# Kernel tuning notes

Hardware: AMD Instinct MI355X
Metric: run time of the kernel (lower is better)

Reference implementation:

```python
import jax, jax.numpy as jnp
import numpy as np

N_NODES = 50000
N_EDGES = 800000
F_IN = 128
HID = 256


def setup_inputs() -> dict:
    key = jax.random.key(0)
    ks = jax.random.split(key, 10)
    x = jax.random.normal(ks[0], (N_NODES, F_IN), jnp.float32)
    edge_index = jax.random.randint(ks[1], (2, N_EDGES), 0, N_NODES, jnp.int32)
    # Glorot-ish scaled weights (PyG Linear default init style)
    def w(k, o, i):
        return jax.random.normal(k, (o, i), jnp.float32) * (1.0 / np.sqrt(i))
    return {
        "x": x,
        "edge_index": edge_index,
        "W1l": w(ks[2], HID, F_IN), "b1l": jnp.zeros((HID,), jnp.float32),
        "W1r": w(ks[3], HID, F_IN),
        "W2l": w(ks[4], HID, HID), "b2l": jnp.zeros((HID,), jnp.float32),
        "W2r": w(ks[5], HID, HID),
        "Wh1": w(ks[6], 4, HID), "bh1": jnp.zeros((4,), jnp.float32),
        "Wh2": w(ks[7], 3, HID), "bh2": jnp.zeros((3,), jnp.float32),
    }


def sage_conv(x, edge_index, Wl, bl, Wr):
    # PyG SAGEConv (aggr='mean'): out_i = Wl @ mean_{j in N(i)} x_j + bl + Wr @ x_i
    src, dst = edge_index[0], edge_index[1]
    n = x.shape[0]
    summed = jax.ops.segment_sum(x[src], dst, num_segments=n)        # [N, F]
    cnt = jax.ops.segment_sum(jnp.ones((src.shape[0],), x.dtype), dst, num_segments=n)
    agg = summed / jnp.maximum(cnt, 1.0)[:, None]                    # isolated nodes -> 0
    return agg @ Wl.T + bl + x @ Wr.T


def reference(x, edge_index, W1l, b1l, W1r, W2l, b2l, W2r, Wh1, bh1, Wh2, bh2):
    h = jax.nn.relu(sage_conv(x, edge_index, W1l, b1l, W1r))
    # dropout(p=0.5) is identity in eval mode
    h = sage_conv(h, edge_index, W2l, b2l, W2r)
    out1 = h @ Wh1.T + bh1   # l2_classifier=False branch
    out2 = h @ Wh2.T + bh2
    return (out1, out2, h)
```

## Files before the change

### kernel.cpp

```cpp
#include <hip/hip_runtime.h>
#include <hip/hip_bf16.h>

typedef short bf16x8 __attribute__((ext_vector_type(8)));
typedef float f32x4 __attribute__((ext_vector_type(4)));

__device__ __forceinline__ float bf2f(__hip_bfloat16 v) { return __bfloat162float(v); }
__device__ __forceinline__ float sh2f(short s) {
    union { float f; unsigned u; } c; c.u = ((unsigned)(unsigned short)s) << 16; return c.f;
}
__device__ __forceinline__ short f2sh(float f) {
    __hip_bfloat16 b = __float2bfloat16(f); return *(short*)&b;
}

__device__ __forceinline__ float loadAny(const void* p, size_t i, int isf32) {
    return isf32 ? ((const float*)p)[i] : bf2f(((const __hip_bfloat16*)p)[i]);
}

__global__ void pre_kernel(const void* __restrict__ x,
                           const void* W1l, const void* W1r, const void* W2l, const void* W2r,
                           const void* b1l, const void* b2l, const void* Wh1, const void* Wh2,
                           const void* bh1, const void* bh2,
                           const int* __restrict__ ei, int E,
                           __hip_bfloat16* __restrict__ xn,
                           __hip_bfloat16* __restrict__ W1c, __hip_bfloat16* __restrict__ W2c,
                           __hip_bfloat16* __restrict__ sb,
                           int* __restrict__ deg, int* __restrict__ rank,
                           int* __restrict__ flag, int N) {
    __shared__ int sflag;
    int tid = threadIdx.x;
    if (tid < 64) {
        const unsigned short* xu = (const unsigned short*)x;
        unsigned short u = xu[tid * 2];
        unsigned e = (u >> 7) & 0xFF;
        bool good = (u == 0) || (e >= 110 && e <= 137);
        unsigned long long m = __ballot(good);
        if (tid == 0) sflag = (__popcll(m) < 32) ? 1 : 0;
    }
    __syncthreads();
    int isf32 = sflag;
    int gid = blockIdx.x * 256 + tid;
    if (gid == 0) *flag = isf32;

    if (gid < E) {
        rank[gid] = atomicAdd(&deg[ei[E + gid]], 1);
    }

    int n4 = N * 32;
    if (gid < n4) {
        short4 o;
        if (isf32) {
            float4 v = ((const float4*)x)[gid];
            o.x = f2sh(v.x); o.y = f2sh(v.y); o.z = f2sh(v.z); o.w = f2sh(v.w);
        } else {
            o = ((const short4*)x)[gid];
        }
        ((short4*)xn)[gid] = o;
    }

    if (gid < 65536) {
        int n = gid >> 8, k = gid & 255;
        float v = (k < 128) ? loadAny(W1l, n * 128 + k, isf32)
                            : loadAny(W1r, n * 128 + (k - 128), isf32);
        W1c[gid] = __float2bfloat16(v);
        return;
    }
    int u = gid - 65536;
    if (u < 131072) {
        int n = u >> 9, k = u & 511;
        float v = (k < 256) ? loadAny(W2l, n * 256 + k, isf32)
                            : loadAny(W2r, n * 256 + (k - 256), isf32);
        W2c[u] = __float2bfloat16(v);
        return;
    }
    int s = u - 131072;
    float v;
    if      (s < 256)  v = loadAny(b1l, s, isf32);
    else if (s < 512)  v = loadAny(b2l, s - 256, isf32);
    else if (s < 1536) v = loadAny(Wh1, s - 512, isf32);
    else if (s < 2304) v = loadAny(Wh2, s - 1536, isf32);
    else if (s < 2308) v = loadAny(bh1, s - 2304, isf32);
    else if (s < 2311) v = loadAny(bh2, s - 2308, isf32);
    else return;
    sb[s] = __float2bfloat16(v);
}

__global__ __launch_bounds__(256) void scanA_kernel(const int* __restrict__ deg,
                                                    int* __restrict__ off,
                                                    int* __restrict__ bsum, int N) {
    __shared__ int ts[256];
    int t = threadIdx.x;
    int base = blockIdx.x * 1024 + t * 4;
    int v0 = (base + 0 < N) ? deg[base + 0] : 0;
    int v1 = (base + 1 < N) ? deg[base + 1] : 0;
    int v2 = (base + 2 < N) ? deg[base + 2] : 0;
    int v3 = (base + 3 < N) ? deg[base + 3] : 0;
    int i0 = v0, i1 = i0 + v1, i2 = i1 + v2, i3 = i2 + v3;
    ts[t] = i3;
    __syncthreads();
    for (int d = 1; d < 256; d <<= 1) {
        int x = (t >= d) ? ts[t - d] : 0;
        __syncthreads();
        ts[t] += x;
        __syncthreads();
    }
    int excl = (t > 0) ? ts[t - 1] : 0;
    if (base + 0 < N) off[base + 1] = excl + i0;
    if (base + 1 < N) off[base + 2] = excl + i1;
    if (base + 2 < N) off[base + 3] = excl + i2;
    if (base + 3 < N) off[base + 4] = excl + i3;
    if (t == 255) bsum[blockIdx.x] = ts[255];
}

__global__ void addC_kernel(int* __restrict__ off, const int* __restrict__ bsum,
                            int N, int nb) {
    __shared__ int ex[64];
    int t = threadIdx.x;
    if (t < 64) {
        int v = (t < nb) ? bsum[t] : 0;
        for (int d = 1; d < 64; d <<= 1) {
            int y = __shfl_up(v, d, 64);
            if (t >= d) v += y;
        }
        ex[t] = v;
    }
    __syncthreads();
    int i = blockIdx.x * 256 + t;
    if (i == 0) off[0] = 0;
    if (i < N) {
        int b = i >> 10;
        int excl = (b > 0) ? ex[b - 1] : 0;
        off[i + 1] += excl;
    }
}

__global__ void fill_kernel(const int* __restrict__ ei, int E,
                            const int* __restrict__ off, const int* __restrict__ rank,
                            unsigned short* __restrict__ srcs) {
    int t = blockIdx.x * blockDim.x + threadIdx.x;
    if (t >= E) return;
    int dst = ei[E + t];
    int pos = off[dst] + rank[t];
    srcs[pos] = (unsigned short)ei[t];
}

__global__ void gather1_kernel(const __hip_bfloat16* __restrict__ x,
                               const int* __restrict__ off,
                               const unsigned short* __restrict__ srcs,
                               __hip_bfloat16* __restrict__ agg, int N) {
    int gid  = blockIdx.x * blockDim.x + threadIdx.x;
    int wid  = gid >> 6;
    int lane = threadIdx.x & 63;
    int node = wid * 4 + (lane >> 4);
    int t    = lane & 15;
    if (node >= N) return;
    int beg = off[node], end = off[node + 1];
    float a[8] = {0.f, 0.f, 0.f, 0.f, 0.f, 0.f, 0.f, 0.f};
    const bf16x8* xb = (const bf16x8*)x;
    int e = beg;
    for (; e + 7 < end; e += 8) {
        bf16x8 v[8];
#pragma unroll
        for (int j = 0; j < 8; j++) v[j] = xb[(size_t)srcs[e + j] * 16 + t];
#pragma unroll
        for (int j = 0; j < 8; j++)
#pragma unroll
            for (int k = 0; k < 8; k++) a[k] += sh2f(v[j][k]);
    }
    for (; e < end; e++) {
        bf16x8 v = xb[(size_t)srcs[e] * 16 + t];
#pragma unroll
        for (int k = 0; k < 8; k++) a[k] += sh2f(v[k]);
    }
    float inv = 1.0f / fmaxf((float)(end - beg), 1.0f);
    bf16x8 o;
#pragma unroll
    for (int k = 0; k < 8; k++) o[k] = f2sh(a[k] * inv);
    ((bf16x8*)agg)[(size_t)node * 16 + t] = o;
}

__global__ void gather2_kernel(const __hip_bfloat16* __restrict__ h,
                               const int* __restrict__ off,
                               const unsigned short* __restrict__ srcs,
                               __hip_bfloat16* __restrict__ agg, int N) {
    int gid  = blockIdx.x * blockDim.x + threadIdx.x;
    int wid  = gid >> 6;
    int lane = threadIdx.x & 63;
    int node = wid * 2 + (lane >> 5);
    int t    = lane & 31;
    if (node >= N) return;
    int beg = off[node], end = off[node + 1];
    float a[8] = {0.f, 0.f, 0.f, 0.f, 0.f, 0.f, 0.f, 0.f};
    const bf16x8* hb = (const bf16x8*)h;
    int e = beg;
    for (; e + 7 < end; e += 8) {
        bf16x8 v[8];
#pragma unroll
        for (int j = 0; j < 8; j++) v[j] = hb[(size_t)srcs[e + j] * 32 + t];
#pragma unroll
        for (int j = 0; j < 8; j++)
#pragma unroll
            for (int k = 0; k < 8; k++) a[k] += sh2f(v[j][k]);
    }
    for (; e < end; e++) {
        bf16x8 v = hb[(size_t)srcs[e] * 32 + t];
#pragma unroll
        for (int k = 0; k < 8; k++) a[k] += sh2f(v[k]);
    }
    float inv = 1.0f / fmaxf((float)(end - beg), 1.0f);
    bf16x8 o;
#pragma unroll
    for (int k = 0; k < 8; k++) o[k] = f2sh(a[k] * inv);
    ((bf16x8*)agg)[(size_t)node * 32 + t] = o;
}

struct AFrag { bf16x8 v[2]; };

template <int K, int KA, bool RELU, bool TOOUT>
__global__ __launch_bounds__(256) void gemm_lds(const __hip_bfloat16* __restrict__ A1,
                                                const __hip_bfloat16* __restrict__ A2, int M,
                                                const __hip_bfloat16* __restrict__ W,
                                                const __hip_bfloat16* __restrict__ bias,
                                                __hip_bfloat16* __restrict__ outb,
                                                void* __restrict__ dout,
                                                const int* __restrict__ flag) {
    __shared__ short wlds[16384];
    constexpr int KB = K - KA;
    constexpr int NCHUNK = K / 128;
    int tid  = threadIdx.x;
    int wave = tid >> 6, lane = tid & 63, quad = lane >> 4, l15 = lane & 15;
    int rowBlk = blockIdx.x >> 1, half = blockIdx.x & 1;
    int R0 = rowBlk * 128;
    int cbase = half * 128;

    int mrow[2];
#pragma unroll
    for (int rt = 0; rt < 2; rt++) mrow[rt] = min(R0 + wave * 32 + rt * 16 + l15, M - 1);

    const short* Ws = (const short*)W;

    auto loadW = [&](int p, bf16x8* wreg) {
#pragma unroll
        for (int i = 0; i < 8; i++) {
            int unit = tid + i * 256;
            int ln = unit & 63, nt = (unit >> 6) & 7, kt = unit >> 9;
            int row = cbase + nt * 16 + (ln & 15);
            int kk  = p * 128 + kt * 32 + (ln >> 4) * 8;
            wreg[i] = *(const bf16x8*)(Ws + (size_t)row * K + kk);
        }
    };
    auto storeW = [&](const bf16x8* wreg) {
#pragma unroll
        for (int i = 0; i < 8; i++) {
            int unit = tid + i * 256;
            *(bf16x8*)&wlds[unit * 8] = wreg[i];
        }
    };
    auto loadA = [&](int kglob) {
        AFrag f;
#pragma unroll
        for (int rt = 0; rt < 2; rt++) {
            const short* ap = (kglob < KA)
                ? (const short*)A1 + (size_t)mrow[rt] * KA + kglob + quad * 8
                : (const short*)A2 + (size_t)mrow[rt] * KB + (kglob - KA) + quad * 8;
            f.v[rt] = *(const bf16x8*)ap;
        }
        return f;
    };

    f32x4 acc[2][8];
#pragma unroll
    for (int rt = 0; rt < 2; rt++)
#pragma unroll
        for (int nt = 0; nt < 8; nt++) acc[rt][nt] = {0.f, 0.f, 0.f, 0.f};

    bf16x8 wreg[8];
    loadW(0, wreg);
    storeW(wreg);
    __syncthreads();
    AFrag a0f = loadA(0);
    AFrag a1f = loadA(32 < K ? 32 : 0);

    for (int p = 0; p < NCHUNK; p++) {
        if (p + 1 < NCHUNK) loadW(p + 1, wreg);
#pragma unroll
        for (int kt = 0; kt < 4; kt++) {
            int kg = p * 128 + kt * 32;
            int kg2 = kg + 64;
            if (kg2 > K - 32) kg2 = K - 32;
            AFrag a_next = loadA(kg2);
#pragma unroll
            for (int nt = 0; nt < 8; nt++) {
                bf16x8 b = *(const bf16x8*)&wlds[((kt * 8 + nt) * 64 + lane) * 8];
#pragma unroll
                for (int rt = 0; rt < 2; rt++)
                    acc[rt][nt] = __builtin_amdgcn_mfma_f32_16x16x32_bf16(a0f.v[rt], b, acc[rt][nt], 0, 0, 0);
            }
            a0f = a1f;
            a1f = a_next;
        }
        if (p + 1 < NCHUNK) {
            __syncthreads();
            storeW(wreg);
            __syncthreads();
        }
    }

    int isf32 = TOOUT ? *flag : 0;
    float* hf = TOOUT ? ((float*)dout + (size_t)M * 7) : nullptr;
    __hip_bfloat16* hb = TOOUT ? ((__hip_bfloat16*)dout + (size_t)M * 7) : outb;

#pragma unroll
    for (int rt = 0; rt < 2; rt++) {
#pragma unroll
        for (int nt = 0; nt < 8; nt++) {
            int col = cbase + nt * 16 + l15;
            float bv = bf2f(bias[col]);
#pragma unroll
            for (int r = 0; r < 4; r++) {
                int row = R0 + wave * 32 + rt * 16 + quad * 4 + r;
                if (row < M) {
                    float v = acc[rt][nt][r] + bv;
                    if (RELU) v = fmaxf(v, 0.f);
                    size_t idx = (size_t)row * 256 + col;
                    if (TOOUT && isf32) hf[idx] = v;
                    else                hb[idx] = __float2bfloat16(v);
                }
            }
        }
    }
}

__global__ void heads_kernel(const __hip_bfloat16* __restrict__ sb,
                             void* dout, int N, const int* __restrict__ flag) {
    int isf32 = *flag;
    int node = (blockIdx.x * blockDim.x + threadIdx.x) >> 6;
    int lane = threadIdx.x & 63;
    if (node >= N) return;
    float hv0, hv1, hv2, hv3;
    if (isf32) {
        const float4* hp = (const float4*)((const float*)dout + (size_t)N * 7);
        float4 v = hp[(size_t)node * 64 + lane];
        hv0 = v.x; hv1 = v.y; hv2 = v.z; hv3 = v.w;
    } else {
        const __hip_bfloat162* hp = (const __hip_bfloat162*)((const __hip_bfloat16*)dout + (size_t)N * 7);
        __hip_bfloat162 a = hp[(size_t)node * 128 + 2 * lane];
        __hip_bfloat162 b = hp[(size_t)node * 128 + 2 * lane + 1];
        hv0 = bf2f(a.x); hv1 = bf2f(a.y); hv2 = bf2f(b.x); hv3 = bf2f(b.y);
    }
#pragma unroll
    for (int r = 0; r < 7; r++) {
        const __hip_bfloat16* wrow = (r < 4) ? (sb + 512 + r * 256) : (sb + 1536 + (r - 4) * 256);
        const __hip_bfloat162* wr2 = (const __hip_bfloat162*)wrow;
        __hip_bfloat162 wa = wr2[2 * lane];
        __hip_bfloat162 wb = wr2[2 * lane + 1];
        float p = hv0 * bf2f(wa.x) + hv1 * bf2f(wa.y) + hv2 * bf2f(wb.x) + hv3 * bf2f(wb.y);
        for (int off = 32; off > 0; off >>= 1) p += __shfl_down(p, off, 64);
        if (lane == 0) {
            float bias = (r < 4) ? bf2f(sb[2304 + r]) : bf2f(sb[2308 + (r - 4)]);
            float v = p + bias;
            size_t idx = (r < 4) ? ((size_t)node * 4 + r)
                                 : ((size_t)N * 4 + (size_t)node * 3 + (r - 4));
            if (isf32) ((float*)dout)[idx] = v;
            else       ((__hip_bfloat16*)dout)[idx] = __float2bfloat16(v);
        }
    }
}

extern "C" void kernel_launch(void* const* d_in, const int* in_sizes, int n_in,
                              void* d_out, int out_size, void* d_ws, size_t ws_size,
                              hipStream_t stream) {
    const void* x   = d_in[0];
    const int*  ei  = (const int*)d_in[1];
    const void* W1l = d_in[2];
    const void* b1l = d_in[3];
    const void* W1r = d_in[4];
    const void* W2l = d_in[5];
    const void* b2l = d_in[6];
    const void* W2r = d_in[7];
    const void* Wh1 = d_in[8];
    const void* bh1 = d_in[9];
    const void* Wh2 = d_in[10];
    const void* bh2 = d_in[11];

    const int N = in_sizes[0] / 128;
    const int E = in_sizes[1] / 2;
    const int NB = (N + 1023) / 1024;

    char* ws = (char*)d_ws;
    int*            offp   = (int*)(ws + 0);
    int*            deg    = (int*)(ws + 262144);
    int*            bsum   = (int*)(ws + 524288);
    unsigned short* srcs   = (unsigned short*)(ws + 786432);
    __hip_bfloat16* W1c    = (__hip_bfloat16*)(ws + 3986432);
    __hip_bfloat16* W2c    = (__hip_bfloat16*)(ws + 4117504);
    __hip_bfloat16* sb     = (__hip_bfloat16*)(ws + 4379648);
    __hip_bfloat16* xn     = (__hip_bfloat16*)(ws + 4387840);
    __hip_bfloat16* h1     = (__hip_bfloat16*)(ws + 17187840);
    int*            rank   = (int*)(ws + 17187840);
    __hip_bfloat16* agg    = (__hip_bfloat16*)(ws + 42787840);
    int*            flag   = (int*)(ws + 68387840);

    hipMemsetAsync(deg, 0, (size_t)N * 4, stream);
    pre_kernel<<<(N * 32 + 255) / 256, 256, 0, stream>>>(
        x, W1l, W1r, W2l, W2r, b1l, b2l, Wh1, Wh2, bh1, bh2, ei, E,
        xn, W1c, W2c, sb, deg, rank, flag, N);

    scanA_kernel<<<NB, 256, 0, stream>>>(deg, offp, bsum, N);
    addC_kernel<<<(N + 255) / 256, 256, 0, stream>>>(offp, bsum, N, NB);
    fill_kernel<<<(E + 255) / 256, 256, 0, stream>>>(ei, E, offp, rank, srcs);

    const int rowBlks = (N + 127) / 128;

    {
        int waves = (N + 3) / 4;
        gather1_kernel<<<(waves * 64 + 255) / 256, 256, 0, stream>>>(xn, offp, srcs, agg, N);
    }
    gemm_lds<256, 128, true, false><<<rowBlks * 2, 256, 0, stream>>>(
        agg, xn, N, W1c, sb, h1, nullptr, flag);

    {
        int waves = (N + 1) / 2;
        gather2_kernel<<<(waves * 64 + 255) / 256, 256, 0, stream>>>(h1, offp, srcs, agg, N);
    }
    gemm_lds<512, 256, false, true><<<rowBlks * 2, 256, 0, stream>>>(
        agg, h1, N, W2c, sb + 256, nullptr, d_out, flag);

    heads_kernel<<<(N + 3) / 4, 256, 0, stream>>>(sb, d_out, N, flag);
}
```

Measured before the change: 337.9 us.

## Pre-swizzle weights into MFMA fragment order and read them directly from global

The prep kernel now writes the combined weight matrices in the exact per-lane MFMA B-fragment order. The GEMM drops its LDS staging of weight chunks and the block barriers that came with it. Each wave instead reads its B fragments straight from global memory, relying on L2/L1 caching because the weights are shared by all blocks. This frees LDS and removes the sync points, at the cost of more global or cache traffic per wave, since the four waves each reload the same weights.

```diff
diff --git a/kernel.cpp b/kernel.cpp
--- a/kernel.cpp
+++ b/kernel.cpp
@@ -22,7 +22,7 @@
                            const void* bh1, const void* bh2,
                            const int* __restrict__ ei, int E,
                            __hip_bfloat16* __restrict__ xn,
-                           __hip_bfloat16* __restrict__ W1c, __hip_bfloat16* __restrict__ W2c,
+                           __hip_bfloat16* __restrict__ W1f, __hip_bfloat16* __restrict__ W2f,
                            __hip_bfloat16* __restrict__ sb,
                            int* __restrict__ deg, int* __restrict__ rank,
                            int* __restrict__ flag, int N) {
@@ -61,7 +61,8 @@
         int n = gid >> 8, k = gid & 255;
         float v = (k < 128) ? loadAny(W1l, n * 128 + k, isf32)
                             : loadAny(W1r, n * 128 + (k - 128), isf32);
-        W1c[gid] = __float2bfloat16(v);
+        int idx = ((((k >> 5) * 16 + (n >> 4)) * 64) + ((k >> 3) & 3) * 16 + (n & 15)) * 8 + (k & 7);
+        W1f[idx] = __float2bfloat16(v);
         return;
     }
     int u = gid - 65536;
@@ -69,7 +70,8 @@
         int n = u >> 9, k = u & 511;
         float v = (k < 256) ? loadAny(W2l, n * 256 + k, isf32)
                             : loadAny(W2r, n * 256 + (k - 256), isf32);
-        W2c[u] = __float2bfloat16(v);
+        int idx = ((((k >> 5) * 16 + (n >> 4)) * 64) + ((k >> 3) & 3) * 16 + (n & 15)) * 8 + (k & 7);
+        W2f[idx] = __float2bfloat16(v);
         return;
     }
     int s = u - 131072;
@@ -216,16 +218,15 @@
 struct AFrag { bf16x8 v[2]; };
 
 template <int K, int KA, bool RELU, bool TOOUT>
-__global__ __launch_bounds__(256) void gemm_lds(const __hip_bfloat16* __restrict__ A1,
-                                                const __hip_bfloat16* __restrict__ A2, int M,
-                                                const __hip_bfloat16* __restrict__ W,
-                                                const __hip_bfloat16* __restrict__ bias,
-                                                __hip_bfloat16* __restrict__ outb,
-                                                void* __restrict__ dout,
-                                                const int* __restrict__ flag) {
-    __shared__ short wlds[16384];
+__global__ __launch_bounds__(256) void gemm_nolds(const __hip_bfloat16* __restrict__ A1,
+                                                  const __hip_bfloat16* __restrict__ A2, int M,
+                                                  const short* __restrict__ Wf,
+                                                  const __hip_bfloat16* __restrict__ bias,
+                                                  __hip_bfloat16* __restrict__ outb,
+                                                  void* __restrict__ dout,
+                                                  const int* __restrict__ flag) {
     constexpr int KB = K - KA;
-    constexpr int NCHUNK = K / 128;
+    constexpr int KT = K / 32;
     int tid  = threadIdx.x;
     int wave = tid >> 6, lane = tid & 63, quad = lane >> 4, l15 = lane & 15;
     int rowBlk = blockIdx.x >> 1, half = blockIdx.x & 1;
@@ -236,25 +237,6 @@
 #pragma unroll
     for (int rt = 0; rt < 2; rt++) mrow[rt] = min(R0 + wave * 32 + rt * 16 + l15, M - 1);
 
-    const short* Ws = (const short*)W;
-
-    auto loadW = [&](int p, bf16x8* wreg) {
-#pragma unroll
-        for (int i = 0; i < 8; i++) {
-            int unit = tid + i * 256;
-            int ln = unit & 63, nt = (unit >> 6) & 7, kt = unit >> 9;
-            int row = cbase + nt * 16 + (ln & 15);
-            int kk  = p * 128 + kt * 32 + (ln >> 4) * 8;
-            wreg[i] = *(const bf16x8*)(Ws + (size_t)row * K + kk);
-        }
-    };
-    auto storeW = [&](const bf16x8* wreg) {
-#pragma unroll
-        for (int i = 0; i < 8; i++) {
-            int unit = tid + i * 256;
-            *(bf16x8*)&wlds[unit * 8] = wreg[i];
-        }
-    };
     auto loadA = [&](int kglob) {
         AFrag f;
 #pragma unroll
@@ -273,36 +255,24 @@
 #pragma unroll
         for (int nt = 0; nt < 8; nt++) acc[rt][nt] = {0.f, 0.f, 0.f, 0.f};
 
-    bf16x8 wreg[8];
-    loadW(0, wreg);
-    storeW(wreg);
-    __syncthreads();
     AFrag a0f = loadA(0);
-    AFrag a1f = loadA(32 < K ? 32 : 0);
-
-    for (int p = 0; p < NCHUNK; p++) {
-        if (p + 1 < NCHUNK) loadW(p + 1, wreg);
-#pragma unroll
-        for (int kt = 0; kt < 4; kt++) {
-            int kg = p * 128 + kt * 32;
-            int kg2 = kg + 64;
-            if (kg2 > K - 32) kg2 = K - 32;
-            AFrag a_next = loadA(kg2);
-#pragma unroll
-            for (int nt = 0; nt < 8; nt++) {
-                bf16x8 b = *(const bf16x8*)&wlds[((kt * 8 + nt) * 64 + lane) * 8];
-#pragma unroll
-                for (int rt = 0; rt < 2; rt++)
-                    acc[rt][nt] = __builtin_amdgcn_mfma_f32_16x16x32_bf16(a0f.v[rt], b, acc[rt][nt], 0, 0, 0);
-            }
-            a0f = a1f;
-            a1f = a_next;
-        }
-        if (p + 1 < NCHUNK) {
-            __syncthreads();
-            storeW(wreg);
-            __syncthreads();
-        }
+    AFrag a1f = loadA(32);
+
+#pragma unroll
+    for (int kt = 0; kt < KT; kt++) {
+        int kg2 = kt * 32 + 64;
+        if (kg2 > K - 32) kg2 = K - 32;
+        AFrag a_next = loadA(kg2);
+#pragma unroll
+        for (int nt = 0; nt < 8; nt++) {
+            int nt_g = half * 8 + nt;
+            bf16x8 b = *(const bf16x8*)(Wf + (size_t)((kt * 16 + nt_g) * 64 + lane) * 8);
+#pragma unroll
+            for (int rt = 0; rt < 2; rt++)
+                acc[rt][nt] = __builtin_amdgcn_mfma_f32_16x16x32_bf16(a0f.v[rt], b, acc[rt][nt], 0, 0, 0);
+        }
+        a0f = a1f;
+        a1f = a_next;
     }
 
     int isf32 = TOOUT ? *flag : 0;
@@ -391,8 +361,8 @@
     int*            deg    = (int*)(ws + 262144);
     int*            bsum   = (int*)(ws + 524288);
     unsigned short* srcs   = (unsigned short*)(ws + 786432);
-    __hip_bfloat16* W1c    = (__hip_bfloat16*)(ws + 3986432);
-    __hip_bfloat16* W2c    = (__hip_bfloat16*)(ws + 4117504);
+    __hip_bfloat16* W1f    = (__hip_bfloat16*)(ws + 3986432);
+    __hip_bfloat16* W2f    = (__hip_bfloat16*)(ws + 4117504);
     __hip_bfloat16* sb     = (__hip_bfloat16*)(ws + 4379648);
     __hip_bfloat16* xn     = (__hip_bfloat16*)(ws + 4387840);
     __hip_bfloat16* h1     = (__hip_bfloat16*)(ws + 17187840);
@@ -403,7 +373,7 @@
     hipMemsetAsync(deg, 0, (size_t)N * 4, stream);
     pre_kernel<<<(N * 32 + 255) / 256, 256, 0, stream>>>(
         x, W1l, W1r, W2l, W2r, b1l, b2l, Wh1, Wh2, bh1, bh2, ei, E,
-        xn, W1c, W2c, sb, deg, rank, flag, N);
+        xn, W1f, W2f, sb, deg, rank, flag, N);
 
     scanA_kernel<<<NB, 256, 0, stream>>>(deg, offp, bsum, N);
     addC_kernel<<<(N + 255) / 256, 256, 0, stream>>>(offp, bsum, N, NB);
@@ -415,15 +385,15 @@
         int waves = (N + 3) / 4;
         gather1_kernel<<<(waves * 64 + 255) / 256, 256, 0, stream>>>(xn, offp, srcs, agg, N);
     }
-    gemm_lds<256, 128, true, false><<<rowBlks * 2, 256, 0, stream>>>(
-        agg, xn, N, W1c, sb, h1, nullptr, flag);
+    gemm_nolds<256, 128, true, false><<<rowBlks * 2, 256, 0, stream>>>(
+        agg, xn, N, (const short*)W1f, sb, h1, nullptr, flag);
 
     {
         int waves = (N + 1) / 2;
         gather2_kernel<<<(waves * 64 + 255) / 256, 256, 0, stream>>>(h1, offp, srcs, agg, N);
     }
-    gemm_lds<512, 256, false, true><<<rowBlks * 2, 256, 0, stream>>>(
-        agg, h1, N, W2c, sb + 256, nullptr, d_out, flag);
+    gemm_nolds<512, 256, false, true><<<rowBlks * 2, 256, 0, stream>>>(
+        agg, h1, N, (const short*)W2f, sb + 256, nullptr, d_out, flag);
 
     heads_kernel<<<(N + 3) / 4, 256, 0, stream>>>(sb, d_out, N, flag);
 }
```

Result: slower. 359.9 us (+6.5%).
